# Performance work log

Measured on AMD Instinct MI355X. Metric: run time of the kernel, lower is better.

Reference implementation:

```python
import jax, jax.numpy as jnp
import numpy as np

SEQ, D_IN, H, D_OUT = 8192, 256, 2048, 64


def setup_inputs() -> dict:
    key = jax.random.key(0)
    ks = jax.random.split(key, 9)
    s = 1.0 / np.sqrt(H)  # torch LSTM/Linear init scale
    u = lambda k, shape: jax.random.uniform(k, shape, jnp.float32, -s, s)
    return {
        "x": jax.random.normal(ks[0], (SEQ, D_IN), jnp.float32),
        "hprev": jax.random.normal(ks[1], (1, 1, H), jnp.float32),
        "cprev": jax.random.normal(ks[2], (1, 1, H), jnp.float32),
        "W_ih": u(ks[3], (4 * H, D_IN)),   # gate order: i, f, g, o
        "W_hh": u(ks[4], (4 * H, H)),
        "b_ih": u(ks[5], (4 * H,)),
        "b_hh": u(ks[6], (4 * H,)),
        "W_fc": u(ks[7], (D_OUT, H)),
        "b_fc": u(ks[8], (D_OUT,)),
    }


def _lstm_forward(x, h0, c0, W_ih, W_hh, b_ih, b_hh, W_fc, b_fc):
    # precompute input contributions for all timesteps: [T, 4H]
    xg = x @ W_ih.T + (b_ih + b_hh)
    W_hh_T = W_hh.T  # [H, 4H]

    def step(carry, xg_t):
        h, c = carry
        z = xg_t + h @ W_hh_T  # [4H]
        i, f, g, o = jnp.split(z, 4)
        i = jax.nn.sigmoid(i)
        f = jax.nn.sigmoid(f)
        g = jnp.tanh(g)
        o = jax.nn.sigmoid(o)
        c = f * c + i * g
        h = o * jnp.tanh(c)
        return (h, c), h

    (hT, cT), hs = jax.lax.scan(step, (h0, c0), xg)
    out = jax.nn.sigmoid(hs @ W_fc.T + b_fc)  # [T, D_OUT]
    return out, hT, cT


def reference(x, hprev, cprev, W_ih, W_hh, b_ih, b_hh, W_fc, b_fc):
    out, hT, cT = _lstm_forward(
        x, hprev[0, 0], cprev[0, 0], W_ih, W_hh, b_ih, b_hh, W_fc, b_fc
    )
    return out, hT[None, None, :], cT[None, None, :]
```

## Files before the change

### kernel.cpp

```cpp
#include <hip/hip_runtime.h>
#include <stdint.h>

typedef __fp16 f16x2 __attribute__((ext_vector_type(2)));
typedef __fp16 f16x8 __attribute__((ext_vector_type(8)));
typedef unsigned long long ull;

#define SEQ  8192
#define HDIM 2048
#define DIN  256
#define DOUT 64
#define NREP 4

__device__ __forceinline__ f16x2 pk(float lo, float hi) {
    return __builtin_amdgcn_cvt_pkrtz(lo, hi);
}
__device__ __forceinline__ f16x2 pk2(float2 v) { return pk(v.x, v.y); }
__device__ __forceinline__ uint32_t h2u(f16x2 h) { return __builtin_bit_cast(uint32_t, h); }
__device__ __forceinline__ float sigf(float x) { return 1.0f / (1.0f + __expf(-x)); }
__device__ __forceinline__ float tanh_fast(float x) { return 2.0f * sigf(2.0f * x) - 1.0f; }

__device__ __forceinline__ int skH(int j) { return j + 4 * (j >> 7); }
__device__ __forceinline__ int skX(int j) { return j + 4 * (j >> 4); }

__global__ void __launch_bounds__(256, 1)
lstm_persist(const float2* __restrict__ x2,
             const float2* __restrict__ hprev2,
             const float*  __restrict__ cprev,
             const float*  __restrict__ wih,
             const float*  __restrict__ whh,
             const float*  __restrict__ bih,
             const float*  __restrict__ bhh,
             const float2* __restrict__ wfc2,
             const float*  __restrict__ bfc,
             float* __restrict__ out,
             uint32_t* __restrict__ hs_w,
             ull* __restrict__ htag)
{
    const int tid = threadIdx.x;
    const int b   = blockIdx.x;
    const int wv  = tid >> 6;
    const int l   = tid & 63;
    const int g   = l >> 4;
    const int p   = (l >> 3) & 1;
    const int c   = l & 7;

    __shared__ __align__(16) uint32_t smem[12672];
    uint32_t* ldsH0 = smem;
    uint32_t* ldsH1 = smem + 1056;
    uint32_t* ldsX  = smem + 2112;
    uint32_t* hsl = smem;
    uint32_t* wfl = smem + 4224;

    uint32_t* hs_priv = hs_w + (size_t)b * 32 * 1024;

    const int unit = 8 * b + 2 * wv + p;
    const int r    = g * 2048 + unit;
    f16x2 wh[128];
    {
        const float4* ptr = (const float4*)(whh + (size_t)r * 2048 + 256 * c);
#pragma unroll
        for (int q = 0; q < 64; ++q) {
            float4 v = ptr[q];
            wh[2*q+0] = pk(v.x, v.y);
            wh[2*q+1] = pk(v.z, v.w);
        }
    }
    f16x2 wx[16];
    {
        const float4* ptr = (const float4*)(wih + (size_t)r * 256 + 32 * c);
#pragma unroll
        for (int q = 0; q < 8; ++q) {
            float4 v = ptr[q];
            wx[2*q+0] = pk(v.x, v.y);
            wx[2*q+1] = pk(v.z, v.w);
        }
    }
#pragma unroll
    for (int k = 0; k < 4; ++k) {
        int j = tid + 256 * k;
        ldsH0[skH(j)] = h2u(pk2(hprev2[j]));
    }
    if (tid < 128) ldsX[skX(tid)] = h2u(pk2(x2[tid]));

    float cloc = cprev[unit];
    float hloc = 0.f;
    const float bsum = bih[r] + bhh[r];
    const ull deadline = __builtin_amdgcn_s_memrealtime() + 60000000ull;
    __syncthreads();

    for (int t = 0; t < SEQ; ++t) {
        uint32_t* ldsH = (t & 1) ? ldsH1 : ldsH0;

        float accs[8];
#pragma unroll
        for (int q = 0; q < 8; ++q) accs[q] = 0.f;
        {
            const f16x8* xp = (const f16x8*)(ldsX + 20 * c);
#pragma unroll
            for (int q = 0; q < 4; ++q) {
                f16x8 xv = xp[q];
#pragma unroll
                for (int d = 0; d < 4; ++d) {
                    f16x2 hv = {xv[2*d], xv[2*d+1]};
                    int idx = 4 * q + d;
                    accs[idx & 7] = __builtin_amdgcn_fdot2(wx[idx], hv, accs[idx & 7], false);
                }
            }
        }
        float2 xw = {0.f, 0.f};
        const bool xl = (tid < 128) && (t + 1 < SEQ);
        if (xl) xw = x2[(size_t)(t + 1) * 128 + tid];

        if (t > 0) {
            const ull* tag = htag + (size_t)(b & (NREP - 1)) * 2048 + (size_t)(t & 1) * 1024;
            uint32_t pay[4] = {0, 0, 0, 0};
            unsigned got = 0;
            int spins = 0;
            while (got != 0xFu) {
#pragma unroll
                for (int k = 0; k < 4; ++k) {
                    if (!(got & (1u << k))) {
                        ull v = __hip_atomic_load(tag + (tid + 256 * k),
                                                  __ATOMIC_RELAXED, __HIP_MEMORY_SCOPE_AGENT);
                        if ((uint32_t)(v >> 32) == (uint32_t)t) {
                            pay[k] = (uint32_t)v;
                            got |= (1u << k);
                        }
                    }
                }
                if (got != 0xFu) {
                    if (spins++ > 0) {
                        if (__builtin_amdgcn_s_memrealtime() > deadline) got = 0xFu;
                        __builtin_amdgcn_s_sleep(1);
                    }
                }
            }
            const bool save = (((t - 1) >> 5) == b);
#pragma unroll
            for (int k = 0; k < 4; ++k) {
                int j = tid + 256 * k;
                ldsH[skH(j)] = pay[k];
                if (save) hs_priv[(size_t)((t - 1) & 31) * 1024 + j] = pay[k];
            }
        }
        __syncthreads();
        if (xl) ldsX[skX(tid)] = h2u(pk2(xw));

        {
            const f16x8* hp = (const f16x8*)(ldsH + 132 * c);
#pragma unroll
            for (int q = 0; q < 32; ++q) {
                f16x8 hv8 = hp[q];
#pragma unroll
                for (int d = 0; d < 4; ++d) {
                    f16x2 hh = {hv8[2*d], hv8[2*d+1]};
                    int idx = 4 * q + d;
                    accs[idx & 7] = __builtin_amdgcn_fdot2(wh[idx], hh, accs[idx & 7], false);
                }
            }
        }
        float acc = ((accs[0] + accs[1]) + (accs[2] + accs[3]))
                  + ((accs[4] + accs[5]) + (accs[6] + accs[7]));
        acc += __shfl_xor(acc, 1);
        acc += __shfl_xor(acc, 2);
        acc += __shfl_xor(acc, 4);

        float z = acc + bsum;
        const bool isg = (g == 2);
        float s  = sigf(isg ? 2.0f * z : z);
        float val = isg ? (2.0f * s - 1.0f) : s;
        const int p8 = l & 8;
        float iv = __shfl(val, p8 + 0);
        float fv = __shfl(val, p8 + 16);
        float gv = __shfl(val, p8 + 32);
        float ov = __shfl(val, p8 + 48);
        cloc = fv * cloc + iv * gv;
        hloc = ov * tanh_fast(cloc);

        float h0 = __shfl(hloc, 0);
        float h1 = __shfl(hloc, 8);
        uint32_t pay = h2u(pk(h0, h1));
        if (l < NREP) {
            ull tv = ((ull)(uint32_t)(t + 1) << 32) | (ull)pay;
            __hip_atomic_store(htag + (size_t)l * 2048 + (size_t)((t + 1) & 1) * 1024 + 4 * b + wv,
                               tv, __ATOMIC_RELAXED, __HIP_MEMORY_SCOPE_AGENT);
        }
    }

    if ((l & 55) == 0) {
        out[(size_t)SEQ * DOUT + unit - g * 0]       = hloc;
        out[(size_t)SEQ * DOUT + HDIM + unit]        = cloc;
    }

    if (b == 255) {
        const ull* tag = htag + (size_t)(255 & (NREP - 1)) * 2048;
        uint32_t pay[4] = {0, 0, 0, 0};
        unsigned got = 0;
        while (got != 0xFu) {
#pragma unroll
            for (int k = 0; k < 4; ++k) {
                if (!(got & (1u << k))) {
                    ull v = __hip_atomic_load(tag + (tid + 256 * k),
                                              __ATOMIC_RELAXED, __HIP_MEMORY_SCOPE_AGENT);
                    if ((uint32_t)(v >> 32) == 8192u) {
                        pay[k] = (uint32_t)v;
                        got |= (1u << k);
                    }
                }
            }
            if (got != 0xFu) {
                if (__builtin_amdgcn_s_memrealtime() > deadline) got = 0xFu;
                __builtin_amdgcn_s_sleep(1);
            }
        }
#pragma unroll
        for (int k = 0; k < 4; ++k)
            hs_priv[(size_t)31 * 1024 + tid + 256 * k] = pay[k];
    }
    __syncthreads();

    const int cc = tid & 63;
    const int rg = tid >> 6;
    const float bo = bfc[cc];
    float fca[8];
#pragma unroll
    for (int q = 0; q < 8; ++q) fca[q] = 0.f;

    for (int ch = 0; ch < 8; ++ch) {
#pragma unroll
        for (int i = 0; i < 16; ++i) {
            int idx = tid + 256 * i;
            int rr = idx >> 7, kp = idx & 127;
            hsl[rr * 132 + kp] = hs_priv[(size_t)rr * 1024 + ch * 128 + kp];
        }
#pragma unroll
        for (int i = 0; i < 32; ++i) {
            int idx = tid + 256 * i;
            int c2 = idx >> 7, kp = idx & 127;
            wfl[c2 * 132 + kp] = h2u(pk2(wfc2[(size_t)c2 * 1024 + ch * 128 + kp]));
        }
        __syncthreads();
#pragma unroll 4
        for (int k4 = 0; k4 < 32; ++k4) {
            f16x8 wvv = *(const f16x8*)(wfl + cc * 132 + 4 * k4);
#pragma unroll
            for (int q = 0; q < 8; ++q) {
                f16x8 hv = *(const f16x8*)(hsl + (rg * 8 + q) * 132 + 4 * k4);
#pragma unroll
                for (int d = 0; d < 4; ++d) {
                    f16x2 a  = {hv[2*d], hv[2*d+1]};
                    f16x2 bb = {wvv[2*d], wvv[2*d+1]};
                    fca[q] = __builtin_amdgcn_fdot2(a, bb, fca[q], false);
                }
            }
        }
        __syncthreads();
    }
#pragma unroll
    for (int q = 0; q < 8; ++q) {
        size_t row = (size_t)32 * b + rg * 8 + q;
        out[row * DOUT + cc] = sigf(fca[q] + bo);
    }
}

extern "C" void kernel_launch(void* const* d_in, const int* in_sizes, int n_in,
                              void* d_out, int out_size, void* d_ws, size_t ws_size,
                              hipStream_t stream) {
    const float2* x2     = (const float2*)d_in[0];
    const float2* hprev2 = (const float2*)d_in[1];
    const float*  cprev  = (const float*)d_in[2];
    const float*  wih    = (const float*)d_in[3];
    const float*  whh    = (const float*)d_in[4];
    const float*  bih    = (const float*)d_in[5];
    const float*  bhh    = (const float*)d_in[6];
    const float2* wfc2   = (const float2*)d_in[7];
    const float*  bfc    = (const float*)d_in[8];
    float*        out    = (float*)d_out;

    uint32_t* hs_w = (uint32_t*)d_ws;
    ull*      htag = (ull*)((char*)d_ws + (size_t)SEQ * 1024 * 4);

    lstm_persist<<<dim3(256), dim3(256), 0, stream>>>(
        x2, hprev2, cprev, wih, whh, bih, bhh, wfc2, bfc,
        out, hs_w, htag);
}
```

Baseline: 24.08 ms.

## Relay per-step hidden state through per-XCD buffers with one global mailbox

```diff
diff --git a/kernel.cpp b/kernel.cpp
--- a/kernel.cpp
+++ b/kernel.cpp
@@ -3,13 +3,13 @@
 
 typedef __fp16 f16x2 __attribute__((ext_vector_type(2)));
 typedef __fp16 f16x8 __attribute__((ext_vector_type(8)));
+typedef uint32_t u32x4 __attribute__((ext_vector_type(4)));
 typedef unsigned long long ull;
 
 #define SEQ  8192
 #define HDIM 2048
 #define DIN  256
 #define DOUT 64
-#define NREP 4
 
 __device__ __forceinline__ f16x2 pk(float lo, float hi) {
     return __builtin_amdgcn_cvt_pkrtz(lo, hi);
@@ -21,6 +21,24 @@
 
 __device__ __forceinline__ int skH(int j) { return j + 4 * (j >> 7); }
 __device__ __forceinline__ int skX(int j) { return j + 4 * (j >> 4); }
+
+__device__ __forceinline__ void ld32_sc1(const ull* p, u32x4& a, u32x4& b) {
+    asm volatile("global_load_dwordx4 %0, %2, off sc1\n\t"
+                 "global_load_dwordx4 %1, %2, off offset:16 sc1\n\t"
+                 "s_waitcnt vmcnt(0)"
+                 : "=&v"(a), "=&v"(b) : "v"(p) : "memory");
+}
+__device__ __forceinline__ void ld32_sc0(const ull* p, u32x4& a, u32x4& b) {
+    asm volatile("global_load_dwordx4 %0, %2, off sc0\n\t"
+                 "global_load_dwordx4 %1, %2, off offset:16 sc0\n\t"
+                 "s_waitcnt vmcnt(0)"
+                 : "=&v"(a), "=&v"(b) : "v"(p) : "memory");
+}
+__device__ __forceinline__ void st32_sc0(ull* p, u32x4 a, u32x4 b) {
+    asm volatile("global_store_dwordx4 %2, %0, off sc0\n\t"
+                 "global_store_dwordx4 %2, %1, off offset:16 sc0"
+                 :: "v"(a), "v"(b), "v"(p) : "memory");
+}
 
 __global__ void __launch_bounds__(256, 1)
 lstm_persist(const float2* __restrict__ x2,
@@ -34,7 +52,9 @@
              const float*  __restrict__ bfc,
              float* __restrict__ out,
              uint32_t* __restrict__ hs_w,
-             ull* __restrict__ htag)
+             ull* __restrict__ htag,
+             ull* __restrict__ xcdbuf,
+             uint32_t* __restrict__ cnt)
 {
     const int tid = threadIdx.x;
     const int b   = blockIdx.x;
@@ -51,7 +71,17 @@
     uint32_t* hsl = smem;
     uint32_t* wfl = smem + 4224;
 
+    __shared__ int sh_grp, sh_slot;
+
     uint32_t* hs_priv = hs_w + (size_t)b * 32 * 1024;
+
+    if (tid == 0) {
+        uint32_t xcc;
+        asm volatile("s_getreg_b32 %0, hwreg(HW_REG_XCC_ID, 0, 32)" : "=s"(xcc));
+        int gidx = (int)(xcc & 7u);
+        sh_grp  = gidx;
+        sh_slot = (int)atomicAdd(cnt + gidx, 1u);
+    }
 
     const int unit = 8 * b + 2 * wv + p;
     const int r    = g * 2048 + unit;
@@ -87,6 +117,9 @@
     const float bsum = bih[r] + bhh[r];
     const ull deadline = __builtin_amdgcn_s_memrealtime() + 60000000ull;
     __syncthreads();
+    const int  grp   = sh_grp;
+    const bool relay = (sh_slot == 0);
+    bool mb_fb = false;
 
     for (int t = 0; t < SEQ; ++t) {
         uint32_t* ldsH = (t & 1) ? ldsH1 : ldsH0;
@@ -112,36 +145,42 @@
         if (xl) xw = x2[(size_t)(t + 1) * 128 + tid];
 
         if (t > 0) {
-            const ull* tag = htag + (size_t)(b & (NREP - 1)) * 2048 + (size_t)(t & 1) * 1024;
-            uint32_t pay[4] = {0, 0, 0, 0};
-            unsigned got = 0;
-            int spins = 0;
-            while (got != 0xFu) {
-#pragma unroll
-                for (int k = 0; k < 4; ++k) {
-                    if (!(got & (1u << k))) {
-                        ull v = __hip_atomic_load(tag + (tid + 256 * k),
-                                                  __ATOMIC_RELAXED, __HIP_MEMORY_SCOPE_AGENT);
-                        if ((uint32_t)(v >> 32) == (uint32_t)t) {
-                            pay[k] = (uint32_t)v;
-                            got |= (1u << k);
-                        }
-                    }
-                }
-                if (got != 0xFu) {
+            const int par = t & 1;
+            u32x4 qa, qb;
+            const ull* mb = htag + (size_t)par * 1024 + 4 * tid;
+            if (relay) {
+                int spins = 0;
+                for (;;) {
+                    ld32_sc1(mb, qa, qb);
+                    if (qa[1] == (uint32_t)t && qa[3] == (uint32_t)t &&
+                        qb[1] == (uint32_t)t && qb[3] == (uint32_t)t) break;
                     if (spins++ > 0) {
-                        if (__builtin_amdgcn_s_memrealtime() > deadline) got = 0xFu;
+                        if (__builtin_amdgcn_s_memrealtime() > deadline) break;
                         __builtin_amdgcn_s_sleep(1);
                     }
                 }
-            }
-            const bool save = (((t - 1) >> 5) == b);
-#pragma unroll
-            for (int k = 0; k < 4; ++k) {
-                int j = tid + 256 * k;
-                ldsH[skH(j)] = pay[k];
-                if (save) hs_priv[(size_t)((t - 1) & 31) * 1024 + j] = pay[k];
-            }
+                st32_sc0(xcdbuf + ((size_t)grp * 2 + par) * 1024 + 4 * tid, qa, qb);
+            } else {
+                const ull* xb = xcdbuf + ((size_t)grp * 2 + par) * 1024 + 4 * tid;
+                int spins = 0;
+                for (;;) {
+                    if (!mb_fb) ld32_sc0(xb, qa, qb);
+                    else        ld32_sc1(mb, qa, qb);
+                    if (qa[1] == (uint32_t)t && qa[3] == (uint32_t)t &&
+                        qb[1] == (uint32_t)t && qb[3] == (uint32_t)t) break;
+                    ++spins;
+                    if (!mb_fb) {
+                        if (spins > 64) mb_fb = true;
+                    } else {
+                        if (__builtin_amdgcn_s_memrealtime() > deadline) break;
+                        __builtin_amdgcn_s_sleep(1);
+                    }
+                }
+            }
+            u32x4 pays = {qa[0], qa[2], qb[0], qb[2]};
+            *(u32x4*)(ldsH + skH(4 * tid)) = pays;
+            if (((t - 1) >> 5) == b)
+                *(u32x4*)(hs_priv + (size_t)((t - 1) & 31) * 1024 + 4 * tid) = pays;
         }
         __syncthreads();
         if (xl) ldsX[skX(tid)] = h2u(pk2(xw));
@@ -180,27 +219,26 @@
         float h0 = __shfl(hloc, 0);
         float h1 = __shfl(hloc, 8);
         uint32_t pay = h2u(pk(h0, h1));
-        if (l < NREP) {
+        if (l == 0) {
             ull tv = ((ull)(uint32_t)(t + 1) << 32) | (ull)pay;
-            __hip_atomic_store(htag + (size_t)l * 2048 + (size_t)((t + 1) & 1) * 1024 + 4 * b + wv,
+            __hip_atomic_store(htag + (size_t)((t + 1) & 1) * 1024 + 4 * b + wv,
                                tv, __ATOMIC_RELAXED, __HIP_MEMORY_SCOPE_AGENT);
         }
     }
 
-    if ((l & 55) == 0) {
-        out[(size_t)SEQ * DOUT + unit - g * 0]       = hloc;
-        out[(size_t)SEQ * DOUT + HDIM + unit]        = cloc;
+    if (l == 0 || l == 8) {
+        out[(size_t)SEQ * DOUT + unit]        = hloc;
+        out[(size_t)SEQ * DOUT + HDIM + unit] = cloc;
     }
 
     if (b == 255) {
-        const ull* tag = htag + (size_t)(255 & (NREP - 1)) * 2048;
         uint32_t pay[4] = {0, 0, 0, 0};
         unsigned got = 0;
         while (got != 0xFu) {
 #pragma unroll
             for (int k = 0; k < 4; ++k) {
                 if (!(got & (1u << k))) {
-                    ull v = __hip_atomic_load(tag + (tid + 256 * k),
+                    ull v = __hip_atomic_load(htag + (tid + 256 * k),
                                               __ATOMIC_RELAXED, __HIP_MEMORY_SCOPE_AGENT);
                     if ((uint32_t)(v >> 32) == 8192u) {
                         pay[k] = (uint32_t)v;
@@ -277,10 +315,14 @@
     const float*  bfc    = (const float*)d_in[8];
     float*        out    = (float*)d_out;
 
-    uint32_t* hs_w = (uint32_t*)d_ws;
-    ull*      htag = (ull*)((char*)d_ws + (size_t)SEQ * 1024 * 4);
-
+    char* ws = (char*)d_ws;
+    uint32_t* hs_w   = (uint32_t*)ws;
+    ull*      htag   = (ull*)(ws + 33554432);
+    ull*      xcdbuf = (ull*)(ws + 33554432 + 16384);
+    uint32_t* cnt    = (uint32_t*)(ws + 33554432 + 16384 + 131072);
+
+    hipMemsetAsync(cnt, 0, 32, stream);
     lstm_persist<<<dim3(256), dim3(256), 0, stream>>>(
         x2, hprev2, cprev, wih, whh, bih, bhh, wfc2, bfc,
-        out, hs_w, htag);
-}
+        out, hs_w, htag, xcdbuf, cnt);
+}
```

New measurement: 31.56 ms. 1.31x slower.
